# Performance work log

Hardware: AMD Instinct MI355X
Metric: run time of the kernel (lower is better)

## Reference

```python
import jax, jax.numpy as jnp
import numpy as np

GRID = 64
DX = 1.0 / GRID            # grid spacing (buffer dx)
RADIUS = 2.5 * DX          # search_radius = dx * 2.5
CIN, COUT = 16, 16
B, N = 2, 8192
EPS = 1e-12
FOUR_OVER_PI = 4.0 / np.pi


def _safe_sqrt(v):
    return jnp.sqrt(jnp.maximum(v, EPS))


def _sphere_to_cylinder(x, y, z):
    # volume-preserving map: unit ball -> cylinder (radius 1, height 2)
    sq = x * x + y * y + z * z
    norm = _safe_sqrt(sq)
    xy2 = x * x + y * y
    cap = 1.25 * z * z > xy2                      # polar-cap region
    s_cap = jnp.sqrt(3.0 * norm / (norm + jnp.abs(z) + EPS))
    s_side = norm / _safe_sqrt(xy2)
    xc = jnp.where(cap, x * s_cap, x * s_side)
    yc = jnp.where(cap, y * s_cap, y * s_side)
    zc = jnp.where(cap, jnp.sign(z) * norm, 1.5 * z)
    zero = sq <= EPS
    z0 = jnp.zeros_like(x)
    return (jnp.where(zero, z0, xc), jnp.where(zero, z0, yc), jnp.where(zero, z0, zc))


def _cylinder_to_cube(x, y, z):
    # area-preserving disc -> square on the xy cross-section
    xy2 = x * x + y * y
    nxy = _safe_sqrt(xy2)
    xdom = jnp.abs(y) <= jnp.abs(x)
    safe_x = jnp.where(jnp.abs(x) > EPS, x, 1.0)
    safe_y = jnp.where(jnp.abs(y) > EPS, y, 1.0)
    tx = jnp.sign(x) * nxy
    ty = jnp.sign(y) * nxy
    xa, ya = tx, tx * FOUR_OVER_PI * jnp.arctan(y / safe_x)
    xb, yb = ty * FOUR_OVER_PI * jnp.arctan(x / safe_y), ty
    xc = jnp.where(xdom, xa, xb)
    yc = jnp.where(xdom, ya, yb)
    zero = xy2 <= EPS
    z0 = jnp.zeros_like(x)
    return jnp.where(zero, z0, xc), jnp.where(zero, z0, yc), z


def _cconv_forward(input, pos, weights, grid_pos):
    Bb, C, D, H, Wd = input.shape
    Np = pos.shape[1]
    # [B,C,D,H,W] -> [B,D,H,W,C] -> [B,G,C]  (matches permute+view in torch)
    feat = jnp.transpose(input, (0, 2, 3, 4, 1)).reshape(Bb, D * H * Wd, C)
    # fixed 6^3 stencil of candidate grid cells around each point
    off = jnp.arange(6) - 2
    o0, o1, o2 = jnp.meshgrid(off, off, off, indexing='ij')
    offs = jnp.stack([o0, o1, o2], axis=-1).reshape(-1, 3)          # [216,3]
    base = jnp.floor(pos / DX).astype(jnp.int32)                    # [B,N,3]
    cand = base[:, :, None, :] + offs[None, None]                   # [B,N,216,3]
    dims = jnp.array([D, H, Wd])
    in_bounds = jnp.all((cand >= 0) & (cand < dims), axis=-1)       # [B,N,216]
    cc = jnp.clip(cand, 0, dims - 1)
    flat = (cc[..., 0] * H + cc[..., 1]) * Wd + cc[..., 2]          # [B,N,216]
    bidx = jnp.arange(Bb)[:, None, None]
    npos = grid_pos[flat]                                           # [B,N,216,3]
    fg = feat[bidx, flat]                                           # [B,N,216,C]
    rel = npos - pos[:, :, None, :]
    dist2 = jnp.sum(rel * rel, axis=-1)
    valid = in_bounds & (dist2 <= RADIUS * RADIUS)
    # map relative offsets (scaled to the unit ball) to the unit cube
    u = rel / RADIUS
    x, y, z = _sphere_to_cylinder(u[..., 0], u[..., 1], u[..., 2])
    x, y, z = _cylinder_to_cube(x, y, z)
    # linear interpolation of the 3x3x3 kernel, align_corners=True -> coords in [0,2]
    taps = jnp.arange(3, dtype=pos.dtype)
    def hat(c):
        c = jnp.clip((c * 0.5 + 0.5) * 2.0, 0.0, 2.0)
        return jnp.maximum(0.0, 1.0 - jnp.abs(c[..., None] - taps))  # [B,N,216,3]
    w0, w1, w2 = hat(x), hat(y), hat(z)
    w27 = jnp.einsum('bnki,bnkj,bnkl->bnkijl', w0, w1, w2).reshape(Bb, Np, -1, 27)
    w27 = w27 * valid[..., None].astype(w27.dtype)
    # accumulate interpolated features per kernel tap, then apply the kernel
    acc = jnp.einsum('bnkt,bnkc->bntc', w27, fg)                    # [B,N,27,C]
    out = jnp.einsum('bntc,tcd->bnd', acc, weights.reshape(27, C, -1))
    # normalize=True (Open3D default): divide by neighbor count
    count = jnp.sum(valid, axis=-1).astype(out.dtype)
    out = out / jnp.maximum(count, 1.0)[..., None]
    return out


def setup_inputs() -> dict:
    key = jax.random.key(0)
    k1, k2, k3 = jax.random.split(key, 3)
    inp = jax.random.normal(k1, (B, CIN, GRID, GRID, GRID), jnp.float32)
    pos = jax.random.uniform(k2, (B, N, 3), jnp.float32)
    weights = jax.random.normal(k3, (3, 3, 3, CIN, COUT), jnp.float32) * 0.05
    ax = jnp.arange(GRID, dtype=jnp.float32) * DX
    g = jnp.stack(jnp.meshgrid(ax, ax, ax, indexing='ij'), axis=-1).reshape(-1, 3)
    return {"input": inp, "pos": pos, "weights": weights, "grid_pos": g}


def reference(input, pos, weights, grid_pos):
    return _cconv_forward(input, pos, weights, grid_pos)
```

## Files before the change

kernel.cpp:

```cpp
#include <hip/hip_runtime.h>
#include <cstdint>

namespace {
constexpr int kG = 262144;
constexpr int kB = 2;
constexpr int kN = 8192;
constexpr int kPts = kB * kN;
constexpr float kDX = 1.0f / 64.0f;
constexpr float kRad2 = 0.00152587890625f;
constexpr float kInvRad = 25.6f;
constexpr float kEps = 1e-12f;
constexpr float kFourOverPi = 1.27323954473516268615f;

constexpr int PPB = 4;
constexpr int THREADS = PPB * 64;
constexpr int MAXREC = 88;
constexpr int SLOT = 12;
constexpr int NFLAT = 108;
constexpr int GSTRIDE = MAXREC * SLOT + NFLAT + 4;
}

__device__ __forceinline__ float sgnf(float v) {
    return (v > 0.f) ? 1.f : ((v < 0.f) ? -1.f : 0.f);
}

__global__ __launch_bounds__(256) void transpose_feat_k(const float* __restrict__ in,
                                                        float* __restrict__ feat) {
    int idx = blockIdx.x * 256 + threadIdx.x;
    if (idx >= kB * kG) return;
    int b = idx >> 18;
    int g = idx & (kG - 1);
    float v[16];
#pragma unroll
    for (int c = 0; c < 16; ++c) v[c] = in[((size_t)(b * 16 + c)) * kG + g];
    float4* dst = reinterpret_cast<float4*>(feat + (size_t)idx * 16);
    dst[0] = make_float4(v[0], v[1], v[2], v[3]);
    dst[1] = make_float4(v[4], v[5], v[6], v[7]);
    dst[2] = make_float4(v[8], v[9], v[10], v[11]);
    dst[3] = make_float4(v[12], v[13], v[14], v[15]);
}

__global__ __launch_bounds__(THREADS) void cconv_main(
    const float* __restrict__ input, const float* __restrict__ pos,
    const float* __restrict__ W, const float* __restrict__ feat,
    float* __restrict__ out, int use_feat)
{
    __shared__ __align__(16) float rec[PPB * GSTRIDE];

    const int tid = threadIdx.x;
    const int wv = tid >> 6;
    const int lane = tid & 63;
    const int sg = lane >> 4;
    const int lig = lane & 15;
    const int pt = blockIdx.x * PPB + wv;
    const int b = pt >> 13;

    const float px = pos[pt * 3 + 0];
    const float py = pos[pt * 3 + 1];
    const float pz = pos[pt * 3 + 2];
    const int bx = (int)floorf(px * 64.f);
    const int by = (int)floorf(py * 64.f);
    const int bz = (int)floorf(pz * 64.f);

    float* grec = rec + wv * GSTRIDE;
    int* iflats = reinterpret_cast<int*>(grec + MAXREC * SLOT);
    int nv = 0;

#pragma unroll
    for (int it = 0; it < 4; ++it) {
        int k = it * 64 + lane;
        bool valid = false;
        float rx = 0.f, ry = 0.f, rz = 0.f;
        int flat16 = 0;
        if (k < 216) {
            int a = k / 36;
            int r = k - a * 36;
            int b1 = r / 6;
            int c1 = r - b1 * 6;
            int g0 = bx + a - 2, g1 = by + b1 - 2, g2 = bz + c1 - 2;
            bool inb = (g0 >= 0) & (g0 < 64) & (g1 >= 0) & (g1 < 64) &
                       (g2 >= 0) & (g2 < 64);
            int q0 = min(max(g0, 0), 63);
            int q1 = min(max(g1, 0), 63);
            int q2 = min(max(g2, 0), 63);
            flat16 = ((q0 * 64 + q1) * 64 + q2) << 4;
            rx = __fsub_rn((float)q0 * kDX, px);
            ry = __fsub_rn((float)q1 * kDX, py);
            rz = __fsub_rn((float)q2 * kDX, pz);
            float d2 = __fadd_rn(__fadd_rn(__fmul_rn(rx, rx), __fmul_rn(ry, ry)),
                                 __fmul_rn(rz, rz));
            valid = inb && (d2 <= kRad2);
        }
        unsigned long long ball = __ballot(valid);
        if (valid) {
            int slot = nv + __popcll(ball & ((1ull << lane) - 1ull));
            *reinterpret_cast<float4*>(grec + slot * SLOT) =
                make_float4(rx, ry, rz, 0.f);
            iflats[slot] = flat16;
        }
        nv += (int)__popcll(ball);
    }
    __builtin_amdgcn_wave_barrier();

    if (lane < 8 && nv + lane < MAXREC) {
        float4 z = make_float4(0.f, 0.f, 0.f, 0.f);
        float4* zp = reinterpret_cast<float4*>(grec + (nv + lane) * SLOT);
        zp[0] = z; zp[1] = z; zp[2] = z;
    }
    if (lane < 24 && nv + lane < NFLAT) iflats[nv + lane] = 0;
    __builtin_amdgcn_wave_barrier();

    const float* fbp = use_feat ? (feat + (size_t)b * kG * 16)
                                : (input + (size_t)b * 16 * kG);
    int fl0 = iflats[sg];
    int fl1 = iflats[sg + 4];
    int fl2 = iflats[sg + 8];
    int fl3 = iflats[sg + 12];
    float f0 = use_feat ? fbp[(size_t)fl0 + lig] : fbp[(size_t)lig * kG + (fl0 >> 4)];
    float f1 = use_feat ? fbp[(size_t)fl1 + lig] : fbp[(size_t)lig * kG + (fl1 >> 4)];
    float f2 = use_feat ? fbp[(size_t)fl2 + lig] : fbp[(size_t)lig * kG + (fl2 >> 4)];
    float f3 = use_feat ? fbp[(size_t)fl3 + lig] : fbp[(size_t)lig * kG + (fl3 >> 4)];

    for (int s = lane; s < nv; s += 64) {
        float* rp = grec + s * SLOT;
        float4 rc = *reinterpret_cast<const float4*>(rp);
        float ux = rc.x * kInvRad, uy = rc.y * kInvRad, uz = rc.z * kInvRad;

        float xx = ux * ux, yy = uy * uy, zz = uz * uz;
        float xy2 = xx + yy;
        float sq = xy2 + zz;
        float nrm = __builtin_amdgcn_sqrtf(fmaxf(sq, kEps));
        bool cap = (1.25f * zz > xy2);
        float scap = __builtin_amdgcn_sqrtf(3.f * nrm) *
                     __builtin_amdgcn_rsqf(nrm + fabsf(uz) + kEps);
        float sside = nrm * __builtin_amdgcn_rsqf(fmaxf(xy2, kEps));
        float sc = cap ? scap : sside;
        float xc = ux * sc, yc = uy * sc;
        float zc = cap ? sgnf(uz) * nrm : 1.5f * uz;
        if (sq <= kEps) { xc = 0.f; yc = 0.f; zc = 0.f; }

        float xy2b = xc * xc + yc * yc;
        float nxy = __builtin_amdgcn_sqrtf(fmaxf(xy2b, kEps));
        bool xdom = (fabsf(yc) <= fabsf(xc));
        float num = xdom ? yc : xc;
        float den = xdom ? xc : yc;
        float dsafe = (fabsf(den) > kEps) ? den : 1.0f;
        float r = num * __builtin_amdgcn_rcpf(dsafe);
        float r2 = r * r;
        float at = -0.01172120f;
        at = at * r2 + 0.05265332f;
        at = at * r2 - 0.11643287f;
        at = at * r2 + 0.19354346f;
        at = at * r2 - 0.33262347f;
        at = at * r2 + 0.99997726f;
        at = at * r;
        float tt = sgnf(den) * nxy;
        float g = tt * kFourOverPi * at;
        float xo = xdom ? tt : g;
        float yo = xdom ? g : tt;
        if (xy2b <= kEps) { xo = 0.f; yo = 0.f; }
        float zo = zc;

        float tx = fminf(fmaxf(xo + 1.f, 0.f), 2.f) - 1.f;
        float ty = fminf(fmaxf(yo + 1.f, 0.f), 2.f) - 1.f;
        float tz = fminf(fmaxf(zo + 1.f, 0.f), 2.f) - 1.f;
        float wx0 = fmaxf(0.f, -tx), wx1 = 1.f - fabsf(tx), wx2 = fmaxf(0.f, tx);
        float wy0 = fmaxf(0.f, -ty), wy1 = 1.f - fabsf(ty), wy2 = fmaxf(0.f, ty);
        float wz0 = fmaxf(0.f, -tz), wz1 = 1.f - fabsf(tz);

        float4* rp4 = reinterpret_cast<float4*>(rp);
        rp4[0] = make_float4(wx0 * wy0, wx0 * wy1, wx0 * wy2, wx1 * wy0);
        rp4[1] = make_float4(wx1 * wy1, wx1 * wy2, wx2 * wy0, wx2 * wy1);
        rp4[2] = make_float4(wx2 * wy2, wz0, wz1, 0.f);
    }
    __builtin_amdgcn_wave_barrier();

    float acc[28];
#pragma unroll
    for (int t = 0; t < 28; ++t) acc[t] = 0.f;

    const int nvp = (nv + 3) & ~3;
    const float* rp = grec + sg * SLOT;
    float4 F0 = reinterpret_cast<const float4*>(rp)[0];
    float4 F1 = reinterpret_cast<const float4*>(rp)[1];
    float4 F2 = reinterpret_cast<const float4*>(rp)[2];

    for (int s = sg; s < nvp; s += 4) {
        const float* rpn = rp + 4 * SLOT;
        float4 G0 = reinterpret_cast<const float4*>(rpn)[0];
        float4 G1 = reinterpret_cast<const float4*>(rpn)[1];
        float4 G2 = reinterpret_cast<const float4*>(rpn)[2];
        int fln = iflats[s + 16];
        float fnew = use_feat ? fbp[(size_t)fln + lig]
                              : fbp[(size_t)lig * kG + (fln >> 4)];

        float wz2 = (1.f - F2.y) - F2.z;
        float m0 = F2.y * f0, m1 = F2.z * f0, m2 = wz2 * f0;
        acc[0]  += F0.x * m0; acc[1]  += F0.x * m1; acc[2]  += F0.x * m2;
        acc[3]  += F0.y * m0; acc[4]  += F0.y * m1; acc[5]  += F0.y * m2;
        acc[6]  += F0.z * m0; acc[7]  += F0.z * m1; acc[8]  += F0.z * m2;
        acc[9]  += F0.w * m0; acc[10] += F0.w * m1; acc[11] += F0.w * m2;
        acc[12] += F1.x * m0; acc[13] += F1.x * m1; acc[14] += F1.x * m2;
        acc[15] += F1.y * m0; acc[16] += F1.y * m1; acc[17] += F1.y * m2;
        acc[18] += F1.z * m0; acc[19] += F1.z * m1; acc[20] += F1.z * m2;
        acc[21] += F1.w * m0; acc[22] += F1.w * m1; acc[23] += F1.w * m2;
        acc[24] += F2.x * m0; acc[25] += F2.x * m1; acc[26] += F2.x * m2;

        f0 = f1; f1 = f2; f2 = f3; f3 = fnew;
        F0 = G0; F1 = G1; F2 = G2; rp = rpn;
    }

    const bool hi32 = (lane >= 32);
    float kp[14];
#pragma unroll
    for (int j = 0; j < 14; ++j) {
        float send = hi32 ? acc[j] : acc[14 + j];
        float recv = __shfl_xor(send, 32);
        kp[j] = (hi32 ? acc[14 + j] : acc[j]) + recv;
    }
    const bool hi16 = (lane & 16) != 0;
    float kk[7];
#pragma unroll
    for (int j = 0; j < 7; ++j) {
        float send = hi16 ? kp[j] : kp[7 + j];
        float recv = __shfl_xor(send, 16);
        kk[j] = (hi16 ? kp[7 + j] : kp[j]) + recv;
    }

    float partial[16];
#pragma unroll
    for (int d = 0; d < 16; ++d) partial[d] = 0.f;
    const float* wbase = W + (sg * 7) * 256 + lig * 16;
#pragma unroll
    for (int j = 0; j < 7; ++j) {
        if (sg * 7 + j < 27) {
            const float4* wr = reinterpret_cast<const float4*>(wbase + j * 256);
            float4 a0 = wr[0], a1 = wr[1], a2 = wr[2], a3 = wr[3];
            float at_ = kk[j];
            partial[0]  += at_ * a0.x; partial[1]  += at_ * a0.y;
            partial[2]  += at_ * a0.z; partial[3]  += at_ * a0.w;
            partial[4]  += at_ * a1.x; partial[5]  += at_ * a1.y;
            partial[6]  += at_ * a1.z; partial[7]  += at_ * a1.w;
            partial[8]  += at_ * a2.x; partial[9]  += at_ * a2.y;
            partial[10] += at_ * a2.z; partial[11] += at_ * a2.w;
            partial[12] += at_ * a3.x; partial[13] += at_ * a3.y;
            partial[14] += at_ * a3.z; partial[15] += at_ * a3.w;
        }
    }

#pragma unroll
    for (int half = 8; half >= 1; half >>= 1) {
        bool up = (lig & half) != 0;
#pragma unroll
        for (int j = 0; j < half; ++j) {
            float send = up ? partial[j] : partial[j + half];
            float recv = __shfl_xor(send, half);
            partial[j] = (up ? partial[j + half] : partial[j]) + recv;
        }
    }
    float res = partial[0];
    res += __shfl_xor(res, 16);
    res += __shfl_xor(res, 32);
    res = res / fmaxf((float)nv, 1.f);
    if (lane < 16) out[(size_t)pt * 16 + lig] = res;
}

extern "C" void kernel_launch(void* const* d_in, const int* in_sizes, int n_in,
                              void* d_out, int out_size, void* d_ws, size_t ws_size,
                              hipStream_t stream) {
    const float* input = (const float*)d_in[0];
    const float* pos   = (const float*)d_in[1];
    const float* W     = (const float*)d_in[2];
    float* out  = (float*)d_out;
    float* feat = (float*)d_ws;

    const size_t feat_bytes = (size_t)kB * kG * 16 * sizeof(float);
    int use_feat = (d_ws != nullptr && ws_size >= feat_bytes) ? 1 : 0;

    if (use_feat) {
        transpose_feat_k<<<(kB * kG + 255) / 256, 256, 0, stream>>>(input, feat);
    }
    cconv_main<<<kPts / PPB, THREADS, 0, stream>>>(input, pos, W, feat, out, use_feat);
}
```

Baseline: 79.62 us.

## Unroll accumulation loop with packed FMA and deeper feature prefetch

The per-record accumulation loop is replaced by a fully unrolled sequence of up to six 16-record blocks. It uses packed two-wide FMAs (v2f) for the 27-tap accumulation and prefetches feature values two blocks ahead (eight in-flight loads instead of four). Record buffers are resized to 96 and zero-padded to the full capacity so the unrolled blocks read clean data. This aims to hide gather latency and halve FMA issue count, at the cost of more registers and a hard cap of 96 neighbors.

```diff
diff --git a/kernel.cpp b/kernel.cpp
--- a/kernel.cpp
+++ b/kernel.cpp
@@ -1,5 +1,7 @@
 #include <hip/hip_runtime.h>
 #include <cstdint>
+
+typedef float v2f __attribute__((ext_vector_type(2)));
 
 namespace {
 constexpr int kG = 262144;
@@ -14,10 +16,10 @@
 
 constexpr int PPB = 4;
 constexpr int THREADS = PPB * 64;
-constexpr int MAXREC = 88;
+constexpr int MAXREC = 96;
 constexpr int SLOT = 12;
-constexpr int NFLAT = 108;
-constexpr int GSTRIDE = MAXREC * SLOT + NFLAT + 4;
+constexpr int NFLAT = 96;
+constexpr int GSTRIDE = MAXREC * SLOT + NFLAT;
 }
 
 __device__ __forceinline__ float sgnf(float v) {
@@ -102,24 +104,22 @@
     }
     __builtin_amdgcn_wave_barrier();
 
-    if (lane < 8 && nv + lane < MAXREC) {
-        float4 z = make_float4(0.f, 0.f, 0.f, 0.f);
-        float4* zp = reinterpret_cast<float4*>(grec + (nv + lane) * SLOT);
-        zp[0] = z; zp[1] = z; zp[2] = z;
-    }
-    if (lane < 24 && nv + lane < NFLAT) iflats[nv + lane] = 0;
+    for (int z = nv + lane; z < MAXREC; z += 64) {
+        float4 zf = make_float4(0.f, 0.f, 0.f, 0.f);
+        float4* zp = reinterpret_cast<float4*>(grec + z * SLOT);
+        zp[0] = zf; zp[1] = zf; zp[2] = zf;
+        iflats[z] = 0;
+    }
     __builtin_amdgcn_wave_barrier();
 
     const float* fbp = use_feat ? (feat + (size_t)b * kG * 16)
                                 : (input + (size_t)b * 16 * kG);
-    int fl0 = iflats[sg];
-    int fl1 = iflats[sg + 4];
-    int fl2 = iflats[sg + 8];
-    int fl3 = iflats[sg + 12];
-    float f0 = use_feat ? fbp[(size_t)fl0 + lig] : fbp[(size_t)lig * kG + (fl0 >> 4)];
-    float f1 = use_feat ? fbp[(size_t)fl1 + lig] : fbp[(size_t)lig * kG + (fl1 >> 4)];
-    float f2 = use_feat ? fbp[(size_t)fl2 + lig] : fbp[(size_t)lig * kG + (fl2 >> 4)];
-    float f3 = use_feat ? fbp[(size_t)fl3 + lig] : fbp[(size_t)lig * kG + (fl3 >> 4)];
+#define LDF(IDX) (use_feat ? fbp[(size_t)iflats[(IDX)] + lig]                 \
+                           : fbp[(size_t)lig * kG + (iflats[(IDX)] >> 4)])
+    float fa0 = LDF(sg),      fa1 = LDF(sg + 4);
+    float fa2 = LDF(sg + 8),  fa3 = LDF(sg + 12);
+    float fb0 = LDF(sg + 16), fb1 = LDF(sg + 20);
+    float fb2 = LDF(sg + 24), fb3 = LDF(sg + 28);
 
     for (int s = lane; s < nv; s += 64) {
         float* rp = grec + s * SLOT;
@@ -175,40 +175,83 @@
     }
     __builtin_amdgcn_wave_barrier();
 
-    float acc[28];
-#pragma unroll
-    for (int t = 0; t < 28; ++t) acc[t] = 0.f;
-
-    const int nvp = (nv + 3) & ~3;
-    const float* rp = grec + sg * SLOT;
-    float4 F0 = reinterpret_cast<const float4*>(rp)[0];
-    float4 F1 = reinterpret_cast<const float4*>(rp)[1];
-    float4 F2 = reinterpret_cast<const float4*>(rp)[2];
-
-    for (int s = sg; s < nvp; s += 4) {
-        const float* rpn = rp + 4 * SLOT;
-        float4 G0 = reinterpret_cast<const float4*>(rpn)[0];
-        float4 G1 = reinterpret_cast<const float4*>(rpn)[1];
-        float4 G2 = reinterpret_cast<const float4*>(rpn)[2];
-        int fln = iflats[s + 16];
-        float fnew = use_feat ? fbp[(size_t)fln + lig]
-                              : fbp[(size_t)lig * kG + (fln >> 4)];
-
-        float wz2 = (1.f - F2.y) - F2.z;
-        float m0 = F2.y * f0, m1 = F2.z * f0, m2 = wz2 * f0;
-        acc[0]  += F0.x * m0; acc[1]  += F0.x * m1; acc[2]  += F0.x * m2;
-        acc[3]  += F0.y * m0; acc[4]  += F0.y * m1; acc[5]  += F0.y * m2;
-        acc[6]  += F0.z * m0; acc[7]  += F0.z * m1; acc[8]  += F0.z * m2;
-        acc[9]  += F0.w * m0; acc[10] += F0.w * m1; acc[11] += F0.w * m2;
-        acc[12] += F1.x * m0; acc[13] += F1.x * m1; acc[14] += F1.x * m2;
-        acc[15] += F1.y * m0; acc[16] += F1.y * m1; acc[17] += F1.y * m2;
-        acc[18] += F1.z * m0; acc[19] += F1.z * m1; acc[20] += F1.z * m2;
-        acc[21] += F1.w * m0; acc[22] += F1.w * m1; acc[23] += F1.w * m2;
-        acc[24] += F2.x * m0; acc[25] += F2.x * m1; acc[26] += F2.x * m2;
-
-        f0 = f1; f1 = f2; f2 = f3; f3 = fnew;
-        F0 = G0; F1 = G1; F2 = G2; rp = rpn;
-    }
+    v2f az0_01 = {0.f, 0.f}, az1_01 = {0.f, 0.f}, az2_01 = {0.f, 0.f};
+    v2f az0_23 = {0.f, 0.f}, az1_23 = {0.f, 0.f}, az2_23 = {0.f, 0.f};
+    v2f az0_45 = {0.f, 0.f}, az1_45 = {0.f, 0.f}, az2_45 = {0.f, 0.f};
+    v2f az0_67 = {0.f, 0.f}, az1_67 = {0.f, 0.f}, az2_67 = {0.f, 0.f};
+    float a8_0 = 0.f, a8_1 = 0.f, a8_2 = 0.f;
+
+    const int nvp16 = (nv + 15) & ~15;
+    const int M = nvp16 >> 4;
+
+#define REC_FMA(S, FV)                                                        \
+  {                                                                           \
+    const float4* rp4_ = reinterpret_cast<const float4*>(grec + (S) * SLOT);  \
+    float4 Wa = rp4_[0], Wb = rp4_[1], Wc = rp4_[2];                          \
+    float m0 = Wc.y * (FV), m1 = Wc.z * (FV);                                 \
+    float m2 = ((1.f - Wc.y) - Wc.z) * (FV);                                  \
+    v2f mz0 = {m0, m0}, mz1 = {m1, m1}, mz2 = {m2, m2};                       \
+    v2f p01 = {Wa.x, Wa.y}, p23 = {Wa.z, Wa.w};                               \
+    v2f p45 = {Wb.x, Wb.y}, p67 = {Wb.z, Wb.w};                               \
+    az0_01 = __builtin_elementwise_fma(p01, mz0, az0_01);                     \
+    az1_01 = __builtin_elementwise_fma(p01, mz1, az1_01);                     \
+    az2_01 = __builtin_elementwise_fma(p01, mz2, az2_01);                     \
+    az0_23 = __builtin_elementwise_fma(p23, mz0, az0_23);                     \
+    az1_23 = __builtin_elementwise_fma(p23, mz1, az1_23);                     \
+    az2_23 = __builtin_elementwise_fma(p23, mz2, az2_23);                     \
+    az0_45 = __builtin_elementwise_fma(p45, mz0, az0_45);                     \
+    az1_45 = __builtin_elementwise_fma(p45, mz1, az1_45);                     \
+    az2_45 = __builtin_elementwise_fma(p45, mz2, az2_45);                     \
+    az0_67 = __builtin_elementwise_fma(p67, mz0, az0_67);                     \
+    az1_67 = __builtin_elementwise_fma(p67, mz1, az1_67);                     \
+    az2_67 = __builtin_elementwise_fma(p67, mz2, az2_67);                     \
+    a8_0 = __builtin_fmaf(Wc.x, m0, a8_0);                                    \
+    a8_1 = __builtin_fmaf(Wc.x, m1, a8_1);                                    \
+    a8_2 = __builtin_fmaf(Wc.x, m2, a8_2);                                    \
+  }
+
+#define P2BODY(KK, F0_, F1_, F2_, F3_)                                        \
+  {                                                                           \
+    const int rb_ = (KK) * 16 + sg;                                           \
+    float nf0_ = 0.f, nf1_ = 0.f, nf2_ = 0.f, nf3_ = 0.f;                     \
+    const bool dol_ = (M > (KK) + 2);                                         \
+    if (dol_) {                                                               \
+      int q0_ = iflats[rb_ + 32], q1_ = iflats[rb_ + 36],                     \
+          q2_ = iflats[rb_ + 40], q3_ = iflats[rb_ + 44];                     \
+      if (use_feat) {                                                         \
+        nf0_ = fbp[(size_t)q0_ + lig]; nf1_ = fbp[(size_t)q1_ + lig];         \
+        nf2_ = fbp[(size_t)q2_ + lig]; nf3_ = fbp[(size_t)q3_ + lig];         \
+      } else {                                                                \
+        nf0_ = fbp[(size_t)lig * kG + (q0_ >> 4)];                            \
+        nf1_ = fbp[(size_t)lig * kG + (q1_ >> 4)];                            \
+        nf2_ = fbp[(size_t)lig * kG + (q2_ >> 4)];                            \
+        nf3_ = fbp[(size_t)lig * kG + (q3_ >> 4)];                            \
+      }                                                                       \
+    }                                                                         \
+    REC_FMA(rb_,      F0_); REC_FMA(rb_ + 4,  F1_);                           \
+    REC_FMA(rb_ + 8,  F2_); REC_FMA(rb_ + 12, F3_);                           \
+    if (dol_) { F0_ = nf0_; F1_ = nf1_; F2_ = nf2_; F3_ = nf3_; }             \
+  }
+
+    if (M > 0) P2BODY(0, fa0, fa1, fa2, fa3)
+    if (M > 1) P2BODY(1, fb0, fb1, fb2, fb3)
+    if (M > 2) P2BODY(2, fa0, fa1, fa2, fa3)
+    if (M > 3) P2BODY(3, fb0, fb1, fb2, fb3)
+    if (M > 4) P2BODY(4, fa0, fa1, fa2, fa3)
+    if (M > 5) P2BODY(5, fb0, fb1, fb2, fb3)
+
+    float acc[28] = {
+        az0_01.x, az1_01.x, az2_01.x,
+        az0_01.y, az1_01.y, az2_01.y,
+        az0_23.x, az1_23.x, az2_23.x,
+        az0_23.y, az1_23.y, az2_23.y,
+        az0_45.x, az1_45.x, az2_45.x,
+        az0_45.y, az1_45.y, az2_45.y,
+        az0_67.x, az1_67.x, az2_67.x,
+        az0_67.y, az1_67.y, az2_67.y,
+        a8_0,     a8_1,     a8_2,
+        0.f
+    };
 
     const bool hi32 = (lane >= 32);
     float kp[14];
@@ -263,6 +306,9 @@
     res += __shfl_xor(res, 32);
     res = res / fmaxf((float)nv, 1.f);
     if (lane < 16) out[(size_t)pt * 16 + lig] = res;
+#undef LDF
+#undef REC_FMA
+#undef P2BODY
 }
 
 extern "C" void kernel_launch(void* const* d_in, const int* in_sizes, int n_in,
```

After: 74.84 us. -6.0%, faster.
